# Optimization experiments

Hardware: AMD Instinct MI355X
Metric: run time of the kernel (lower is better)

Reference implementation:

```python
import jax, jax.numpy as jnp
import numpy as np

N_NODES = 100000
IN_DIM = 512
OUT_DIM = 16
N_EDGES = 3200000


def setup_inputs() -> dict:
    key = jax.random.key(0)
    k1, k2, k3, k4 = jax.random.split(key, 4)
    x = jax.random.normal(k1, (N_NODES, IN_DIM), dtype=jnp.float32)
    edge_index = jax.random.randint(k2, (2, N_EDGES), 0, N_NODES, dtype=jnp.int64)
    # GCNConv params (glorot weight, zero bias as in PyG)
    scale = jnp.sqrt(6.0 / (IN_DIM + OUT_DIM)).astype(jnp.float32)
    W = jax.random.uniform(k3, (IN_DIM, OUT_DIM), dtype=jnp.float32, minval=-scale, maxval=scale)
    b = jnp.zeros((OUT_DIM,), dtype=jnp.float32)
    return {"x": x, "edge_index": edge_index, "W": W, "b": b}


def reference(x, edge_index, W, b):
    n = x.shape[0]
    # GCNConv with normalize=True: add self-loops, symmetric deg normalization
    loops = jnp.arange(n, dtype=edge_index.dtype)
    row = jnp.concatenate([edge_index[0], loops])  # source nodes
    col = jnp.concatenate([edge_index[1], loops])  # target nodes

    h = x @ W  # [N, 16] dense linear transform

    deg = jax.ops.segment_sum(jnp.ones_like(col, dtype=h.dtype), col, num_segments=n)
    dinv = jnp.where(deg > 0, jax.lax.rsqrt(jnp.maximum(deg, 1.0)), 0.0)
    norm = dinv[row] * dinv[col]  # [E+N]

    # gather source features, scale, scatter-add into targets
    out = jax.ops.segment_sum(norm[:, None] * h[row], col, num_segments=n)
    return out + b
```

## Files before the change

### kernel.cpp

```cpp
#include <hip/hip_runtime.h>
#include <hip/hip_fp16.h>

#define IN_DIM 512
#define OUT_DIM 16
#define KC 32
#define TILE_ROWS 256

#define BSHIFT 8
#define BNODES 256
#define MAXBUCK 512
#define BCOUNT_CHUNK 4096
#define BIN_CHUNK 2048

#define GKC 16
__global__ __launch_bounds__(256, 8) void gemm_xw_split(const float* __restrict__ x,
                                                        const float* __restrict__ W,
                                                        const int* __restrict__ hist,
                                                        __half* __restrict__ hp, int n) {
    __shared__ float xs[4 * 64 * (GKC + 1)];
    const int tid = threadIdx.x;
    const int r = tid & 63;
    const int q = __builtin_amdgcn_readfirstlane(tid >> 6);
    const int rbase = blockIdx.x * 64;
    const int myrow = rbase + r;

    float acc[OUT_DIM];
#pragma unroll
    for (int j = 0; j < OUT_DIM; ++j) acc[j] = 0.f;

    for (int c = 0; c < 8; ++c) {
        __syncthreads();
#pragma unroll
        for (int i = 0; i < 4; ++i) {
            const int v = tid + 256 * i;
            const int row = v >> 4;
            const int qq = (v >> 2) & 3;
            const int f4 = (v & 3) << 2;
            if (rbase + row < n) {
                const float4 f = *(const float4*)(x + (size_t)(rbase + row) * IN_DIM
                                                  + qq * 128 + c * GKC + f4);
                float* d = xs + qq * (64 * (GKC + 1)) + row * (GKC + 1) + f4;
                d[0] = f.x; d[1] = f.y; d[2] = f.z; d[3] = f.w;
            }
        }
        __syncthreads();

        const float* xrow = xs + q * (64 * (GKC + 1)) + r * (GKC + 1);
        const float* Wb = W + (size_t)(q * 128 + c * GKC) * OUT_DIM;
#pragma unroll 4
        for (int k = 0; k < GKC; ++k) {
            const float xv = xrow[k];
            const float* wr = Wb + k * OUT_DIM;
            const float4 w0 = *(const float4*)(wr + 0);
            const float4 w1 = *(const float4*)(wr + 4);
            const float4 w2 = *(const float4*)(wr + 8);
            const float4 w3 = *(const float4*)(wr + 12);
            acc[0]  += xv * w0.x; acc[1]  += xv * w0.y; acc[2]  += xv * w0.z; acc[3]  += xv * w0.w;
            acc[4]  += xv * w1.x; acc[5]  += xv * w1.y; acc[6]  += xv * w1.z; acc[7]  += xv * w1.w;
            acc[8]  += xv * w2.x; acc[9]  += xv * w2.y; acc[10] += xv * w2.z; acc[11] += xv * w2.w;
            acc[12] += xv * w3.x; acc[13] += xv * w3.y; acc[14] += xv * w3.z; acc[15] += xv * w3.w;
        }
    }

    __syncthreads();
    float* red = xs;
    if (q > 0) {
        float* d = red + (q - 1) * (64 * 17) + r * 17;
#pragma unroll
        for (int j = 0; j < OUT_DIM; ++j) d[j] = acc[j];
    }
    __syncthreads();
    if (tid < 64 && myrow < n) {
        const float* p0 = red + 0 * (64 * 17) + tid * 17;
        const float* p1 = red + 1 * (64 * 17) + tid * 17;
        const float* p2 = red + 2 * (64 * 17) + tid * 17;
        const float s = rsqrtf((float)(hist[myrow] + 1));
        __half2* op = (__half2*)(hp + (size_t)myrow * OUT_DIM);
#pragma unroll
        for (int j = 0; j < 8; ++j) {
            const float lo = acc[2 * j]     + p0[2 * j]     + p1[2 * j]     + p2[2 * j];
            const float hi = acc[2 * j + 1] + p0[2 * j + 1] + p1[2 * j + 1] + p2[2 * j + 1];
            op[j] = __floats2half2_rn(s * lo, s * hi);
        }
    }
}

__global__ __launch_bounds__(256) void gemm_xw(const float* __restrict__ x,
                                               const float* __restrict__ W,
                                               const int* __restrict__ hist,
                                               __half* __restrict__ hp, int n) {
    __shared__ float xs[TILE_ROWS * (KC + 1)];
    const int tid = threadIdx.x;
    const int rbase = blockIdx.x * TILE_ROWS;
    const int myrow = rbase + tid;

    float acc[OUT_DIM];
#pragma unroll
    for (int j = 0; j < OUT_DIM; ++j) acc[j] = 0.f;

    for (int kc = 0; kc < IN_DIM; kc += KC) {
        __syncthreads();
#pragma unroll
        for (int i = 0; i < 8; ++i) {
            const int v = tid + 256 * i;
            const int r = v >> 3;
            const int c = (v & 7) << 2;
            if (rbase + r < n) {
                const float4 f = *(const float4*)(x + (size_t)(rbase + r) * IN_DIM + kc + c);
                float* d = xs + r * (KC + 1) + c;
                d[0] = f.x; d[1] = f.y; d[2] = f.z; d[3] = f.w;
            }
        }
        __syncthreads();

        const float* xrow = xs + tid * (KC + 1);
#pragma unroll 4
        for (int k = 0; k < KC; ++k) {
            const float xv = xrow[k];
            const float* wr = W + (size_t)(kc + k) * OUT_DIM;
            const float4 w0 = *(const float4*)(wr + 0);
            const float4 w1 = *(const float4*)(wr + 4);
            const float4 w2 = *(const float4*)(wr + 8);
            const float4 w3 = *(const float4*)(wr + 12);
            acc[0]  += xv * w0.x; acc[1]  += xv * w0.y; acc[2]  += xv * w0.z; acc[3]  += xv * w0.w;
            acc[4]  += xv * w1.x; acc[5]  += xv * w1.y; acc[6]  += xv * w1.z; acc[7]  += xv * w1.w;
            acc[8]  += xv * w2.x; acc[9]  += xv * w2.y; acc[10] += xv * w2.z; acc[11] += xv * w2.w;
            acc[12] += xv * w3.x; acc[13] += xv * w3.y; acc[14] += xv * w3.z; acc[15] += xv * w3.w;
        }
    }

    if (myrow < n) {
        const float s = rsqrtf((float)(hist[myrow] + 1));
        __half2* op = (__half2*)(hp + (size_t)myrow * OUT_DIM);
#pragma unroll
        for (int j = 0; j < 8; ++j)
            op[j] = __floats2half2_rn(s * acc[2 * j], s * acc[2 * j + 1]);
    }
}

__device__ inline void scan512_excl(const int* src, int* dst, int lane) {
    int c[8], pre[8];
    int tot = 0;
#pragma unroll
    for (int k = 0; k < 8; ++k) { c[k] = src[lane * 8 + k]; pre[k] = tot; tot += c[k]; }
    int incl = tot;
#pragma unroll
    for (int d = 1; d < 64; d <<= 1) {
        const int u = __shfl_up(incl, d);
        if (lane >= d) incl += u;
    }
    const int excl = incl - tot;
#pragma unroll
    for (int k = 0; k < 8; ++k) dst[lane * 8 + k] = excl + pre[k];
}

__device__ inline void scan256_excl(const int* src, int* dst, int lane) {
    int c[4], pre[4];
    int tot = 0;
#pragma unroll
    for (int k = 0; k < 4; ++k) { c[k] = src[lane * 4 + k]; pre[k] = tot; tot += c[k]; }
    int incl = tot;
#pragma unroll
    for (int d = 1; d < 64; d <<= 1) {
        const int u = __shfl_up(incl, d);
        if (lane >= d) incl += u;
    }
    const int excl = incl - tot;
#pragma unroll
    for (int k = 0; k < 4; ++k) dst[lane * 4 + k] = excl + pre[k];
}

__global__ __launch_bounds__(256) void bcount(const int* __restrict__ dst,
                                              int* __restrict__ bcnt, int E, int nbuck) {
    __shared__ int lhist[MAXBUCK];
    const int tid = threadIdx.x;
    for (int i = tid; i < MAXBUCK; i += 256) lhist[i] = 0;
    __syncthreads();

    const int base = blockIdx.x * BCOUNT_CHUNK + tid * 16;
#pragma unroll
    for (int g = 0; g < 4; ++g) {
        const int e = base + g * 4;
        if (e + 3 < E) {
            const int4 d = *(const int4*)(dst + e);
            atomicAdd(&lhist[d.x >> BSHIFT], 1);
            atomicAdd(&lhist[d.y >> BSHIFT], 1);
            atomicAdd(&lhist[d.z >> BSHIFT], 1);
            atomicAdd(&lhist[d.w >> BSHIFT], 1);
        } else {
            for (int u = 0; u < 4; ++u)
                if (e + u < E) atomicAdd(&lhist[dst[e + u] >> BSHIFT], 1);
        }
    }
    __syncthreads();
    for (int i = tid; i < nbuck; i += 256)
        if (lhist[i] > 0) atomicAdd(&bcnt[i], lhist[i]);
}

__global__ __launch_bounds__(512) void bucket_scan(const int* __restrict__ bcnt,
                                                   int* __restrict__ bbase,
                                                   int* __restrict__ bcur, int nbuck) {
    __shared__ int sm[MAXBUCK];
    const int t = threadIdx.x;
    sm[t] = (t < nbuck) ? bcnt[t] : 0;
    __syncthreads();
    if (t < 64) scan512_excl(sm, sm, t);
    __syncthreads();
    bbase[t] = sm[t];
    bcur[t] = sm[t];
}

__global__ __launch_bounds__(256) void bin_edges(const int* __restrict__ ei,
                                                 int* __restrict__ bcur,
                                                 int* __restrict__ bins,
                                                 int E, int nbuck) {
    __shared__ int lhist[MAXBUCK];
    __shared__ int lbase[MAXBUCK];
    __shared__ int gbase[MAXBUCK];
    __shared__ int stage[BIN_CHUNK];
    __shared__ short sbkt[BIN_CHUNK];

    const int tid = threadIdx.x;
    const int e0 = blockIdx.x * BIN_CHUNK;
    const int cnt = min(BIN_CHUNK, E - e0);

    for (int i = tid; i < MAXBUCK; i += 256) lhist[i] = 0;
    __syncthreads();

    int myb[8], myr[8], myp[8];
    const int base = e0 + tid * 8;
#pragma unroll
    for (int g = 0; g < 2; ++g) {
        const int e = base + g * 4;
        int ss[4], dd[4];
        if ((E & 3) == 0 && e + 3 < E) {
            const int4 s4 = *(const int4*)(ei + e);
            const int4 d4 = *(const int4*)(ei + (size_t)E + e);
            ss[0] = s4.x; ss[1] = s4.y; ss[2] = s4.z; ss[3] = s4.w;
            dd[0] = d4.x; dd[1] = d4.y; dd[2] = d4.z; dd[3] = d4.w;
        } else {
#pragma unroll
            for (int u = 0; u < 4; ++u) {
                const int idx = e + u;
                ss[u] = (idx < E) ? ei[idx] : -1;
                dd[u] = (idx < E) ? ei[(size_t)E + idx] : 0;
            }
        }
#pragma unroll
        for (int u = 0; u < 4; ++u) {
            const int j = g * 4 + u;
            if (ss[u] >= 0) {
                const int bk = dd[u] >> BSHIFT;
                myb[j] = bk;
                myp[j] = (ss[u] << BSHIFT) | (dd[u] & (BNODES - 1));
                myr[j] = atomicAdd(&lhist[bk], 1);
            } else {
                myb[j] = -1; myr[j] = 0; myp[j] = 0;
            }
        }
    }
    __syncthreads();

    if (tid < 64) scan512_excl(lhist, lbase, tid);
    for (int i = tid; i < nbuck; i += 256)
        if (lhist[i] > 0) gbase[i] = atomicAdd(&bcur[i], lhist[i]);
    __syncthreads();

#pragma unroll
    for (int j = 0; j < 8; ++j) {
        if (myb[j] >= 0) {
            const int p = lbase[myb[j]] + myr[j];
            stage[p] = myp[j];
            sbkt[p] = (short)myb[j];
        }
    }
    __syncthreads();

    for (int i = tid; i < cnt; i += 256) {
        const int bk = sbkt[i];
        bins[gbase[bk] + (i - lbase[bk])] = stage[i];
    }
}

__global__ __launch_bounds__(256) void bucket_sort(const int* __restrict__ bins,
                                                   const int* __restrict__ bbase,
                                                   const int* __restrict__ bcur,
                                                   int* __restrict__ csr,
                                                   int* __restrict__ hist,
                                                   int* __restrict__ off, int n) {
    __shared__ int nhist[BNODES];
    __shared__ int nbase[BNODES];
    __shared__ int ncur[BNODES];
    const int tid = threadIdx.x;
    const int b = blockIdx.x;
    const int s = bbase[b];
    const int e = bcur[b];

    nhist[tid] = 0;
    __syncthreads();
    for (int i = s + tid; i < e; i += 256)
        atomicAdd(&nhist[bins[i] & (BNODES - 1)], 1);
    __syncthreads();
    if (tid < 64) scan256_excl(nhist, nbase, tid);
    __syncthreads();

    const int node = (b << BSHIFT) + tid;
    if (node < n) {
        hist[node] = nhist[tid];
        off[node] = s + nbase[tid];
    }
    ncur[tid] = nbase[tid];
    __syncthreads();

    for (int i = s + tid; i < e; i += 256) {
        const int p = bins[i];
        const int r = atomicAdd(&ncur[p & (BNODES - 1)], 1);
        csr[s + r] = p >> BSHIFT;
    }
}

__global__ __launch_bounds__(256) void gather_out(const int* __restrict__ csr,
                                                  const int* __restrict__ off,
                                                  const int* __restrict__ hist,
                                                  const __half* __restrict__ hp,
                                                  const float* __restrict__ b,
                                                  float* __restrict__ out, int n) {
    const long long gid = (long long)blockIdx.x * 256 + threadIdx.x;
    const int d = (int)(gid >> 3);
    const int j2 = (int)(gid & 7);
    if (d >= n) return;

    const int base = off[d];
    const int deg = hist[d];
    const __half2* hpt = (const __half2*)hp;

    const __half2 sv = hpt[(size_t)d * 8 + j2];
    float ax = __low2float(sv), ay = __high2float(sv);

    int k = 0;
    for (; k + 4 <= deg; k += 4) {
        const int s0 = csr[base + k + 0];
        const int s1 = csr[base + k + 1];
        const int s2 = csr[base + k + 2];
        const int s3 = csr[base + k + 3];
        const __half2 v0 = hpt[(size_t)s0 * 8 + j2];
        const __half2 v1 = hpt[(size_t)s1 * 8 + j2];
        const __half2 v2 = hpt[(size_t)s2 * 8 + j2];
        const __half2 v3 = hpt[(size_t)s3 * 8 + j2];
        ax += __low2float(v0) + __low2float(v1) + __low2float(v2) + __low2float(v3);
        ay += __high2float(v0) + __high2float(v1) + __high2float(v2) + __high2float(v3);
    }
    for (; k < deg; ++k) {
        const __half2 v = hpt[(size_t)csr[base + k] * 8 + j2];
        ax += __low2float(v);
        ay += __high2float(v);
    }

    const float di = rsqrtf((float)(deg + 1));
    float2 o;
    o.x = di * ax + b[2 * j2];
    o.y = di * ay + b[2 * j2 + 1];
    ((float2*)out)[(size_t)d * 8 + j2] = o;
}

__global__ void hist_dst(const int* __restrict__ dst, int* __restrict__ hist, int E) {
    const int t = blockIdx.x * 256 + threadIdx.x;
    const int e0 = t * 4;
    if ((E & 3) == 0 && e0 + 3 < E) {
        const int4 d = *(const int4*)(dst + e0);
        atomicAdd(&hist[d.x], 1);
        atomicAdd(&hist[d.y], 1);
        atomicAdd(&hist[d.z], 1);
        atomicAdd(&hist[d.w], 1);
    } else {
        for (int e = e0; e < E && e < e0 + 4; ++e) atomicAdd(&hist[dst[e]], 1);
    }
}

__global__ __launch_bounds__(256) void scatter_f16(const int* __restrict__ ei,
                                                   const __half* __restrict__ hp,
                                                   __half2* __restrict__ acc, int E) {
    const long long gid = (long long)blockIdx.x * 256 + threadIdx.x;
    const int g = (int)(gid >> 3);
    const int j2 = (int)(gid & 7);
    const int e0 = g * 4;
    if (e0 >= E) return;

    int src[4], dst[4];
#pragma unroll
    for (int u = 0; u < 4; ++u) {
        const int e = e0 + u;
        src[u] = (e < E) ? ei[e] : -1;
        dst[u] = (e < E) ? ei[(size_t)E + e] : -1;
    }
    __half2 v[4];
#pragma unroll
    for (int u = 0; u < 4; ++u)
        if (src[u] >= 0) v[u] = ((const __half2*)(hp + (size_t)src[u] * OUT_DIM))[j2];
#pragma unroll
    for (int u = 0; u < 4; ++u)
        if (dst[u] >= 0) unsafeAtomicAdd(&acc[(size_t)dst[u] * 8 + j2], v[u]);
}

__global__ void finalize(const __half* __restrict__ acc, const __half* __restrict__ hp,
                         const int* __restrict__ hist, const float* __restrict__ b,
                         float* __restrict__ out, int n) {
    const int gid = blockIdx.x * 256 + threadIdx.x;
    if (gid >= n * OUT_DIM) return;
    const int i = gid >> 4;
    const int j = gid & 15;
    const float di = rsqrtf((float)(hist[i] + 1));
    out[gid] = di * (__half2float(acc[gid]) + __half2float(hp[gid])) + b[j];
}


extern "C" void kernel_launch(void* const* d_in, const int* in_sizes, int n_in,
                              void* d_out, int out_size, void* d_ws, size_t ws_size,
                              hipStream_t stream) {
    const float* x  = (const float*)d_in[0];
    const int*   ei = (const int*)d_in[1];
    const float* W  = (const float*)d_in[2];
    const float* b  = (const float*)d_in[3];
    float* out = (float*)d_out;

    const int n = in_sizes[0] / IN_DIM;
    const int E = in_sizes[1] / 2;
    const int nbuck = (n + BNODES - 1) >> BSHIFT;

    __half* hp    = (__half*)d_ws;
    int*    hist  = (int*)(hp + (size_t)n * OUT_DIM);
    int*    off   = hist + n;
    int*    bbase = off + n;
    int*    bcur  = bbase + MAXBUCK;
    int*    bcnt  = bcur + MAXBUCK;
    int*    bins  = bcnt + MAXBUCK;
    int*    csr   = bins + (size_t)E;

    const size_t need = (size_t)n * OUT_DIM * sizeof(__half)
                      + ((size_t)2 * n + 3 * MAXBUCK) * sizeof(int)
                      + 2 * (size_t)E * sizeof(int);

    if (ws_size >= need && nbuck <= MAXBUCK && n < (1 << 23)) {
        hipMemsetAsync(bcnt, 0, MAXBUCK * sizeof(int), stream);

        bcount<<<(E + BCOUNT_CHUNK - 1) / BCOUNT_CHUNK, 256, 0, stream>>>(ei + E, bcnt, E, nbuck);
        bucket_scan<<<1, 512, 0, stream>>>(bcnt, bbase, bcur, nbuck);
        bin_edges<<<(E + BIN_CHUNK - 1) / BIN_CHUNK, 256, 0, stream>>>(ei, bcur, bins, E, nbuck);
        bucket_sort<<<nbuck, 256, 0, stream>>>(bins, bbase, bcur, csr, hist, off, n);
        gemm_xw_split<<<(n + 63) / 64, 256, 0, stream>>>(x, W, hist, hp, n);
        gather_out<<<(int)(((size_t)n * 8 + 255) / 256), 256, 0, stream>>>(csr, off, hist, hp, b, out, n);
    } else {
        __half* acc = (__half*)(hist + n);
        hipMemsetAsync(hist, 0, (size_t)n * sizeof(int), stream);
        hipMemsetAsync(acc, 0, (size_t)n * OUT_DIM * sizeof(__half), stream);

        hist_dst<<<(E + 1023) / 1024, 256, 0, stream>>>(ei + E, hist, E);
        gemm_xw<<<(n + TILE_ROWS - 1) / TILE_ROWS, 256, 0, stream>>>(x, W, hist, hp, n);
        const long long st = ((long long)(E + 3) / 4) * 8;
        scatter_f16<<<(int)((st + 255) / 256), 256, 0, stream>>>(ei, hp, (__half2*)acc, E);
        finalize<<<(n * OUT_DIM + 255) / 256, 256, 0, stream>>>(acc, hp, hist, b, out, n);
    }
}
```

Before: 449.0 us.

## Double-buffer GEMM x tiles in LDS and enlarge edge-binning chunks

The GEMM kernel now prefetches the next K-chunk of x into registers while computing on the current LDS buffer, then writes it to a second LDS buffer. This halves the number of barriers per chunk and hides global load latency. The cost is doubled shared memory and a lower occupancy hint (4 instead of 8). Separately, bin_edges now processes 4096 edges per block, 16 per thread, which cuts the block count and the global atomics on bucket cursors but raises register use.

```diff
diff --git a/kernel.cpp b/kernel.cpp
--- a/kernel.cpp
+++ b/kernel.cpp
@@ -10,42 +10,60 @@
 #define BNODES 256
 #define MAXBUCK 512
 #define BCOUNT_CHUNK 4096
-#define BIN_CHUNK 2048
+#define BIN_CHUNK 4096
 
 #define GKC 16
-__global__ __launch_bounds__(256, 8) void gemm_xw_split(const float* __restrict__ x,
+__global__ __launch_bounds__(256, 4) void gemm_xw_split(const float* __restrict__ x,
                                                         const float* __restrict__ W,
                                                         const int* __restrict__ hist,
                                                         __half* __restrict__ hp, int n) {
-    __shared__ float xs[4 * 64 * (GKC + 1)];
+    __shared__ float xs[2][4 * 64 * (GKC + 1)];
     const int tid = threadIdx.x;
     const int r = tid & 63;
     const int q = __builtin_amdgcn_readfirstlane(tid >> 6);
     const int rbase = blockIdx.x * 64;
     const int myrow = rbase + r;
 
+    int srow[4], sqq[4], sf4[4];
+    bool sok[4];
+#pragma unroll
+    for (int i = 0; i < 4; ++i) {
+        const int v = tid + 256 * i;
+        srow[i] = v >> 4;
+        sqq[i] = (v >> 2) & 3;
+        sf4[i] = (v & 3) << 2;
+        sok[i] = (rbase + srow[i]) < n;
+    }
+    const float* xb = x + (size_t)rbase * IN_DIM;
+
+    float4 st[4];
+#pragma unroll
+    for (int i = 0; i < 4; ++i)
+        if (sok[i])
+            st[i] = *(const float4*)(xb + (size_t)srow[i] * IN_DIM + sqq[i] * 128 + sf4[i]);
+#pragma unroll
+    for (int i = 0; i < 4; ++i)
+        if (sok[i]) {
+            float* d = &xs[0][sqq[i] * (64 * (GKC + 1)) + srow[i] * (GKC + 1) + sf4[i]];
+            d[0] = st[i].x; d[1] = st[i].y; d[2] = st[i].z; d[3] = st[i].w;
+        }
+    __syncthreads();
+
     float acc[OUT_DIM];
 #pragma unroll
     for (int j = 0; j < OUT_DIM; ++j) acc[j] = 0.f;
 
     for (int c = 0; c < 8; ++c) {
-        __syncthreads();
-#pragma unroll
-        for (int i = 0; i < 4; ++i) {
-            const int v = tid + 256 * i;
-            const int row = v >> 4;
-            const int qq = (v >> 2) & 3;
-            const int f4 = (v & 3) << 2;
-            if (rbase + row < n) {
-                const float4 f = *(const float4*)(x + (size_t)(rbase + row) * IN_DIM
-                                                  + qq * 128 + c * GKC + f4);
-                float* d = xs + qq * (64 * (GKC + 1)) + row * (GKC + 1) + f4;
-                d[0] = f.x; d[1] = f.y; d[2] = f.z; d[3] = f.w;
-            }
-        }
-        __syncthreads();
-
-        const float* xrow = xs + q * (64 * (GKC + 1)) + r * (GKC + 1);
+        const int cur = c & 1;
+        if (c < 7) {
+#pragma unroll
+            for (int i = 0; i < 4; ++i)
+                if (sok[i])
+                    st[i] = *(const float4*)(xb + (size_t)srow[i] * IN_DIM
+                                             + sqq[i] * 128 + (c + 1) * GKC + sf4[i]);
+        }
+
+        const float* xrow = &xs[cur][q * (64 * (GKC + 1)) + r * (GKC + 1)];
         const float* Wb = W + (size_t)(q * 128 + c * GKC) * OUT_DIM;
 #pragma unroll 4
         for (int k = 0; k < GKC; ++k) {
@@ -60,10 +78,19 @@
             acc[8]  += xv * w2.x; acc[9]  += xv * w2.y; acc[10] += xv * w2.z; acc[11] += xv * w2.w;
             acc[12] += xv * w3.x; acc[13] += xv * w3.y; acc[14] += xv * w3.z; acc[15] += xv * w3.w;
         }
-    }
-
-    __syncthreads();
-    float* red = xs;
+
+        if (c < 7) {
+#pragma unroll
+            for (int i = 0; i < 4; ++i)
+                if (sok[i]) {
+                    float* d = &xs[cur ^ 1][sqq[i] * (64 * (GKC + 1)) + srow[i] * (GKC + 1) + sf4[i]];
+                    d[0] = st[i].x; d[1] = st[i].y; d[2] = st[i].z; d[3] = st[i].w;
+                }
+        }
+        __syncthreads();
+    }
+
+    float* red = &xs[0][0];
     if (q > 0) {
         float* d = red + (q - 1) * (64 * 17) + r * 17;
 #pragma unroll
@@ -227,10 +254,10 @@
     for (int i = tid; i < MAXBUCK; i += 256) lhist[i] = 0;
     __syncthreads();
 
-    int myb[8], myr[8], myp[8];
-    const int base = e0 + tid * 8;
-#pragma unroll
-    for (int g = 0; g < 2; ++g) {
+    int myb[16], myr[16], myp[16];
+    const int base = e0 + tid * 16;
+#pragma unroll
+    for (int g = 0; g < 4; ++g) {
         const int e = base + g * 4;
         int ss[4], dd[4];
         if ((E & 3) == 0 && e + 3 < E) {
@@ -267,7 +294,7 @@
     __syncthreads();
 
 #pragma unroll
-    for (int j = 0; j < 8; ++j) {
+    for (int j = 0; j < 16; ++j) {
         if (myb[j] >= 0) {
             const int p = lbase[myb[j]] + myr[j];
             stage[p] = myp[j];
```

Result: faster. 420.2 us (-6.4%).
